# Kernel optimization log

Measured on AMD Instinct MI355X. Metric: run time of the kernel, lower is better.

Reference implementation:

```python
import jax, jax.numpy as jnp
import numpy as np

B, N = 256, 4096
IMG_W, IMG_H = 640.0, 480.0


def setup_inputs() -> dict:
    key = jax.random.key(0)
    k0, k1, k2, k3 = jax.random.split(key, 4)
    kpts0 = jax.random.uniform(k0, (B, N, 2), dtype=jnp.float32) * jnp.array([IMG_W, IMG_H], jnp.float32)
    kpts1 = jax.random.uniform(k1, (B, N, 2), dtype=jnp.float32) * jnp.array([IMG_W, IMG_H], jnp.float32)
    conf = jax.random.uniform(k2, (B, N, 1), dtype=jnp.float32)
    t_scale = jax.random.uniform(k3, (B, 2), dtype=jnp.float32) + 0.5
    Kmat = jnp.array([[500.0, 0.0, 320.0], [0.0, 500.0, 240.0], [0.0, 0.0, 1.0]], jnp.float32)
    K = jnp.tile(Kmat[None, None], (B, 2, 1, 1))
    gt_pose_0to1 = jnp.tile(jnp.eye(4, dtype=jnp.float32)[None], (B, 1, 1))
    return {"kpts0": kpts0, "kpts1": kpts1, "conf": conf, "t_scale": t_scale, "K": K, "gt_pose_0to1": gt_pose_0to1}


def _normalize(kpts, Kmat):
    # pixel -> normalized camera coords, homogeneous. kpts:[B,N,2], Kmat:[B,3,3] -> [B,N,3]
    Kinv = jnp.linalg.inv(Kmat)
    h = jnp.concatenate([kpts, jnp.ones_like(kpts[..., :1])], axis=-1)
    return jnp.einsum('bij,bnj->bni', Kinv, h)


def _se3_weighted_8pt(kpts0, kpts1, K0, K1, w, t_scale):
    b_, n_ = kpts0.shape[0], kpts0.shape[1]
    x0 = _normalize(kpts0, K0)  # [B,N,3]
    x1 = _normalize(kpts1, K1)  # [B,N,3]
    # epipolar constraint x1^T E x0 = 0 -> row kron(x1, x0): [B,N,9]
    X = (x1[..., :, None] * x0[..., None, :]).reshape(b_, n_, 9)
    # confidence-weighted normal equations, 9x9 per batch
    M = jnp.einsum('bn,bni,bnj->bij', w, X, X)
    _, V = jnp.linalg.eigh(M)
    E = V[..., 0].reshape(b_, 3, 3)  # eigvec of smallest eigenvalue
    # project to essential manifold + decompose
    U, S, Vt = jnp.linalg.svd(E)
    W = jnp.array([[0.0, -1.0, 0.0], [1.0, 0.0, 0.0], [0.0, 0.0, 1.0]], E.dtype)
    R1 = U @ W @ Vt
    R2 = U @ W.T @ Vt
    R1 = R1 * jnp.sign(jnp.linalg.det(R1))[:, None, None]
    R2 = R2 * jnp.sign(jnp.linalg.det(R2))[:, None, None]
    t = U[..., 2]  # [B,3]
    Rc = jnp.stack([R1, R1, R2, R2], axis=1)   # [B,4,3,3]
    tc = jnp.stack([t, -t, t, -t], axis=1)     # [B,4,3]
    # cheirality: solve d0 * (R x0) - d1 * x1 = -t in least squares (2x2 closed form)
    a = jnp.einsum('bcij,bnj->bcni', Rc, x0)   # [B,4,N,3]
    bvec = x1[:, None]                          # [B,1,N,3]
    tt = tc[:, :, None, :]                      # [B,4,1,3]
    aa = jnp.sum(a * a, -1)
    bb = jnp.sum(bvec * bvec, -1)
    ab = jnp.sum(a * bvec, -1)
    at = jnp.sum(a * tt, -1)
    bt = jnp.sum(bvec * tt, -1)
    det = aa * bb - ab * ab + 1e-9
    d0 = (-at * bb + ab * bt) / det
    d1 = (aa * bt - ab * at) / det
    pos = ((d0 > 0) & (d1 > 0)).astype(w.dtype)
    score = jnp.sum(w[:, None] * pos, -1)       # [B,4]
    best = jnp.argmax(jax.lax.stop_gradient(score), axis=-1)
    oh = jax.nn.one_hot(best, 4, dtype=kpts0.dtype)
    R = jnp.einsum('bc,bcij->bij', oh, Rc)
    t_best = jnp.einsum('bc,bci->bi', oh, tc)
    t_sc = t_best * t_scale[:, None]            # scale unit translation
    top = jnp.concatenate([R, t_sc[..., None]], axis=-1)  # [B,3,4]
    bot = jnp.broadcast_to(jnp.array([0.0, 0.0, 0.0, 1.0], R.dtype), (b_, 1, 4))
    return jnp.concatenate([top, bot], axis=1)  # [B,4,4]


def _se3_inverse(T):
    R = T[:, :3, :3]
    t = T[:, :3, 3:]
    Rt = jnp.swapaxes(R, -1, -2)
    tin = -(Rt @ t)
    top = jnp.concatenate([Rt, tin], axis=-1)
    bot = jnp.broadcast_to(jnp.array([0.0, 0.0, 0.0, 1.0], T.dtype), (T.shape[0], 1, 4))
    return jnp.concatenate([top, bot], axis=1)


def reference(kpts0, kpts1, conf, t_scale, K, gt_pose_0to1):
    w = conf[..., 0]
    T01 = _se3_weighted_8pt(kpts0, kpts1, K[:, 0], K[:, 1], w, t_scale[:, 0])
    T10 = _se3_inverse(T01)
    return jnp.stack([T01, T10], axis=1)  # [B,2,4,4]
```

## Files before the change

kernel.cpp:

```cpp
#include <hip/hip_runtime.h>
#include <math.h>

#define NBATCH 256
#define NPTS   4096
#define NT     256
#define PPT    (NPTS / NT)

__device__ __forceinline__ void inv3x3d(const float* __restrict__ Km, double* Ki) {
  double a = Km[0], bb = Km[1], c = Km[2];
  double d = Km[3], e  = Km[4], f = Km[5];
  double g = Km[6], h  = Km[7], i = Km[8];
  double C00 =  e*i - f*h;
  double C01 = -(d*i - f*g);
  double C02 =  d*h - e*g;
  double det = a*C00 + bb*C01 + c*C02;
  double rd = 1.0/det;
  Ki[0] = C00*rd; Ki[1] = -(bb*i - c*h)*rd; Ki[2] =  (bb*f - c*e)*rd;
  Ki[3] = C01*rd; Ki[4] =  (a*i  - c*g)*rd; Ki[5] = -(a*f  - c*d)*rd;
  Ki[6] = C02*rd; Ki[7] = -(a*h - bb*g)*rd; Ki[8] =  (a*e  - bb*d)*rd;
}

__global__ __launch_bounds__(NT, 1)
void pose_kernel(const float* __restrict__ kpts0,
                 const float* __restrict__ kpts1,
                 const float* __restrict__ conf,
                 const float* __restrict__ t_scale,
                 const float* __restrict__ Kmat,
                 float* __restrict__ out)
{
  const int b    = blockIdx.x;
  const int tid  = threadIdx.x;
  const int lane = tid & 63;
  const int wv   = tid >> 6;

  __shared__ double red[4][45];
  __shared__ double sM[45];
  __shared__ double sR[21];
  __shared__ double sscore[4][4];

  double Ki0[9], Ki1[9];
  inv3x3d(Kmat + (size_t)b*18,     Ki0);
  inv3x3d(Kmat + (size_t)b*18 + 9, Ki1);

  const float2* k0p = (const float2*)kpts0 + (size_t)b*NPTS;
  const float2* k1p = (const float2*)kpts1 + (size_t)b*NPTS;
  const float*  cp  = conf + (size_t)b*NPTS;

  double acc[45];
#pragma unroll
  for (int j=0;j<45;j++) acc[j] = 0.0;

  for (int p=0;p<PPT;p++) {
    const int i = tid + p*NT;
    const float2 q0 = k0p[i];
    const float2 q1 = k1p[i];
    const double w  = (double)cp[i];
    double x0[3], x1[3];
    x0[0] = Ki0[0]*q0.x + Ki0[1]*q0.y + Ki0[2];
    x0[1] = Ki0[3]*q0.x + Ki0[4]*q0.y + Ki0[5];
    x0[2] = Ki0[6]*q0.x + Ki0[7]*q0.y + Ki0[8];
    x1[0] = Ki1[0]*q1.x + Ki1[1]*q1.y + Ki1[2];
    x1[1] = Ki1[3]*q1.x + Ki1[4]*q1.y + Ki1[5];
    x1[2] = Ki1[6]*q1.x + Ki1[7]*q1.y + Ki1[8];
    double X[9];
#pragma unroll
    for (int ii=0; ii<3; ii++)
#pragma unroll
      for (int jj=0; jj<3; jj++)
        X[ii*3+jj] = x1[ii]*x0[jj];
    double wX[9];
#pragma unroll
    for (int j=0;j<9;j++) wX[j] = w*X[j];
    int k = 0;
#pragma unroll
    for (int r=0;r<9;r++)
#pragma unroll
      for (int c=r;c<9;c++) { acc[k] = fma(wX[r], X[c], acc[k]); k++; }
  }

#pragma unroll
  for (int j=0;j<45;j++) {
    double v = acc[j];
#pragma unroll
    for (int off=32; off>0; off>>=1) v += __shfl_xor(v, off, 64);
    acc[j] = v;
  }
  if (lane == 0) {
#pragma unroll
    for (int j=0;j<45;j++) red[wv][j] = acc[j];
  }
  __syncthreads();
  if (tid < 45) sM[tid] = red[0][tid] + red[1][tid] + red[2][tid] + red[3][tid];
  __syncthreads();

  double R1a[9] = {0}, R2a[9] = {0}, ta[3] = {0};
  if (tid == 0) {
    double A[9][9];
#pragma unroll
    for (int r=0;r<9;r++)
#pragma unroll
      for (int c=0;c<9;c++) {
        const int rr = (r<c)?r:c, cc = (r<c)?c:r;
        A[r][c] = sM[rr*9 - (rr*(rr-1))/2 + (cc-rr)];
      }
    double dinv[9];
#pragma unroll
    for (int k=0;k<9;k++) {
      double s = A[k][k];
#pragma unroll
      for (int j=0;j<k;j++) s -= A[k][j]*A[k][j];
      double l = sqrt(fmax(s, 1e-30));
      A[k][k] = l;
      dinv[k] = 1.0/l;
#pragma unroll
      for (int i2=k+1;i2<9;i2++) {
        double s2 = A[i2][k];
#pragma unroll
        for (int j=0;j<k;j++) s2 -= A[i2][j]*A[k][j];
        A[i2][k] = s2*dinv[k];
      }
    }
    double v[9];
#pragma unroll
    for (int j=0;j<9;j++) v[j] = 0.125;
    v[4] = 1.0;
    for (int it=0; it<24; it++) {
      double y[9], z[9];
#pragma unroll
      for (int i2=0;i2<9;i2++) {
        double s = v[i2];
#pragma unroll
        for (int j=0;j<i2;j++) s -= A[i2][j]*y[j];
        y[i2] = s*dinv[i2];
      }
#pragma unroll
      for (int i2=8;i2>=0;i2--) {
        double s = y[i2];
#pragma unroll
        for (int j=i2+1;j<9;j++) s -= A[j][i2]*z[j];
        z[i2] = s*dinv[i2];
      }
      double nn = 0.0;
#pragma unroll
      for (int j=0;j<9;j++) nn += z[j]*z[j];
      double rn = 1.0/sqrt(nn);
#pragma unroll
      for (int j=0;j<9;j++) v[j] = z[j]*rn;
    }
    double E0[3][3];
#pragma unroll
    for (int ii=0;ii<3;ii++)
#pragma unroll
      for (int jj=0;jj<3;jj++) E0[ii][jj] = v[ii*3+jj];
    double G[3][3];
#pragma unroll
    for (int a2=0;a2<3;a2++)
#pragma unroll
      for (int b2=0;b2<3;b2++)
        G[a2][b2] = E0[0][a2]*E0[0][b2] + E0[1][a2]*E0[1][b2] + E0[2][a2]*E0[2][b2];
    double Vv[3][3] = {{1,0,0},{0,1,0},{0,0,1}};
#define JROT(P,Q,RR) do { \
      double apq = G[P][Q]; \
      if (fabs(apq) > 1e-300) { \
        double app = G[P][P], aqq = G[Q][Q]; \
        double tau = (aqq - app) / (2.0*apq); \
        double tt = ((tau >= 0.0) ? 1.0 : -1.0) / (fabs(tau) + sqrt(1.0 + tau*tau)); \
        double cc_ = 1.0/sqrt(1.0 + tt*tt); \
        double ss_ = tt*cc_; \
        G[P][P] = app - tt*apq; \
        G[Q][Q] = aqq + tt*apq; \
        G[P][Q] = 0.0; G[Q][P] = 0.0; \
        double grp = G[RR][P], grq = G[RR][Q]; \
        G[RR][P] = cc_*grp - ss_*grq; G[P][RR] = G[RR][P]; \
        G[RR][Q] = ss_*grp + cc_*grq; G[Q][RR] = G[RR][Q]; \
        double v0p = Vv[0][P], v0q = Vv[0][Q]; \
        Vv[0][P] = cc_*v0p - ss_*v0q; Vv[0][Q] = ss_*v0p + cc_*v0q; \
        double v1p = Vv[1][P], v1q = Vv[1][Q]; \
        Vv[1][P] = cc_*v1p - ss_*v1q; Vv[1][Q] = ss_*v1p + cc_*v1q; \
        double v2p = Vv[2][P], v2q = Vv[2][Q]; \
        Vv[2][P] = cc_*v2p - ss_*v2q; Vv[2][Q] = ss_*v2p + cc_*v2q; \
      } } while(0)
    for (int sw=0; sw<8; sw++) { JROT(0,1,2); JROT(0,2,1); JROT(1,2,0); }
#undef JROT
    double lam[3] = {G[0][0], G[1][1], G[2][2]};
#define CSWAP(A_,B_) if (lam[A_] < lam[B_]) { \
      double tl = lam[A_]; lam[A_] = lam[B_]; lam[B_] = tl; \
      double t0_ = Vv[0][A_]; Vv[0][A_] = Vv[0][B_]; Vv[0][B_] = t0_; \
      double t1_ = Vv[1][A_]; Vv[1][A_] = Vv[1][B_]; Vv[1][B_] = t1_; \
      double t2_ = Vv[2][A_]; Vv[2][A_] = Vv[2][B_]; Vv[2][B_] = t2_; }
    CSWAP(0,1); CSWAP(0,2); CSWAP(1,2);
#undef CSWAP
    double u1[3], u2[3], u3[3];
#pragma unroll
    for (int i3=0;i3<3;i3++)
      u1[i3] = E0[i3][0]*Vv[0][0] + E0[i3][1]*Vv[1][0] + E0[i3][2]*Vv[2][0];
    double n1 = 1.0/sqrt(fmax(u1[0]*u1[0]+u1[1]*u1[1]+u1[2]*u1[2], 1e-300));
#pragma unroll
    for (int i3=0;i3<3;i3++) u1[i3] *= n1;
#pragma unroll
    for (int i3=0;i3<3;i3++)
      u2[i3] = E0[i3][0]*Vv[0][1] + E0[i3][1]*Vv[1][1] + E0[i3][2]*Vv[2][1];
    double d12 = u1[0]*u2[0]+u1[1]*u2[1]+u1[2]*u2[2];
#pragma unroll
    for (int i3=0;i3<3;i3++) u2[i3] -= d12*u1[i3];
    double n2 = 1.0/sqrt(fmax(u2[0]*u2[0]+u2[1]*u2[1]+u2[2]*u2[2], 1e-300));
#pragma unroll
    for (int i3=0;i3<3;i3++) u2[i3] *= n2;
    u3[0] = u1[1]*u2[2] - u1[2]*u2[1];
    u3[1] = u1[2]*u2[0] - u1[0]*u2[2];
    u3[2] = u1[0]*u2[1] - u1[1]*u2[0];
#pragma unroll
    for (int i3=0;i3<3;i3++)
#pragma unroll
      for (int j3=0;j3<3;j3++) {
        double m  = u3[i3]*Vv[j3][2];
        double pA = u2[i3]*Vv[j3][0] - u1[i3]*Vv[j3][1];
        R1a[i3*3+j3] = pA + m;
        R2a[i3*3+j3] = m - pA;
      }
    double det1 = R1a[0]*(R1a[4]*R1a[8]-R1a[5]*R1a[7])
                - R1a[1]*(R1a[3]*R1a[8]-R1a[5]*R1a[6])
                + R1a[2]*(R1a[3]*R1a[7]-R1a[4]*R1a[6]);
    double det2 = R2a[0]*(R2a[4]*R2a[8]-R2a[5]*R2a[7])
                - R2a[1]*(R2a[3]*R2a[8]-R2a[5]*R2a[6])
                + R2a[2]*(R2a[3]*R2a[7]-R2a[4]*R2a[6]);
    double sg1 = (det1 < 0.0) ? -1.0 : 1.0;
    double sg2 = (det2 < 0.0) ? -1.0 : 1.0;
#pragma unroll
    for (int j3=0;j3<9;j3++) { R1a[j3] *= sg1; R2a[j3] *= sg2; }
    ta[0] = u3[0]; ta[1] = u3[1]; ta[2] = u3[2];
#pragma unroll
    for (int j3=0;j3<9;j3++) { sR[j3] = R1a[j3]; sR[9+j3] = R2a[j3]; }
    sR[18] = ta[0]; sR[19] = ta[1]; sR[20] = ta[2];
  }
  __syncthreads();

  double r1[9], r2[9], tv3[3];
#pragma unroll
  for (int j=0;j<9;j++) { r1[j] = sR[j]; r2[j] = sR[9+j]; }
  tv3[0] = sR[18]; tv3[1] = sR[19]; tv3[2] = sR[20];

  double sc[4] = {0.0, 0.0, 0.0, 0.0};
  for (int p=0;p<PPT;p++) {
    const int i = tid + p*NT;
    const float2 q0 = k0p[i];
    const float2 q1 = k1p[i];
    const double w  = (double)cp[i];
    double x0[3], x1[3];
    x0[0] = Ki0[0]*q0.x + Ki0[1]*q0.y + Ki0[2];
    x0[1] = Ki0[3]*q0.x + Ki0[4]*q0.y + Ki0[5];
    x0[2] = Ki0[6]*q0.x + Ki0[7]*q0.y + Ki0[8];
    x1[0] = Ki1[0]*q1.x + Ki1[1]*q1.y + Ki1[2];
    x1[1] = Ki1[3]*q1.x + Ki1[4]*q1.y + Ki1[5];
    x1[2] = Ki1[6]*q1.x + Ki1[7]*q1.y + Ki1[8];
    const double bb2 = x1[0]*x1[0]+x1[1]*x1[1]+x1[2]*x1[2];
    const double bt  = x1[0]*tv3[0]+x1[1]*tv3[1]+x1[2]*tv3[2];
    {
      double a0 = r1[0]*x0[0]+r1[1]*x0[1]+r1[2]*x0[2];
      double a1 = r1[3]*x0[0]+r1[4]*x0[1]+r1[5]*x0[2];
      double a2 = r1[6]*x0[0]+r1[7]*x0[1]+r1[8]*x0[2];
      double aa = a0*a0+a1*a1+a2*a2;
      double ab = a0*x1[0]+a1*x1[1]+a2*x1[2];
      double at = a0*tv3[0]+a1*tv3[1]+a2*tv3[2];
      double n0v = ab*bt - at*bb2;
      double n1v = aa*bt - ab*at;
      if (n0v > 0.0 && n1v > 0.0) sc[0] += w;
      if (n0v < 0.0 && n1v < 0.0) sc[1] += w;
    }
    {
      double a0 = r2[0]*x0[0]+r2[1]*x0[1]+r2[2]*x0[2];
      double a1 = r2[3]*x0[0]+r2[4]*x0[1]+r2[5]*x0[2];
      double a2 = r2[6]*x0[0]+r2[7]*x0[1]+r2[8]*x0[2];
      double aa = a0*a0+a1*a1+a2*a2;
      double ab = a0*x1[0]+a1*x1[1]+a2*x1[2];
      double at = a0*tv3[0]+a1*tv3[1]+a2*tv3[2];
      double n0v = ab*bt - at*bb2;
      double n1v = aa*bt - ab*at;
      if (n0v > 0.0 && n1v > 0.0) sc[2] += w;
      if (n0v < 0.0 && n1v < 0.0) sc[3] += w;
    }
  }
#pragma unroll
  for (int c=0;c<4;c++) {
    double vv = sc[c];
#pragma unroll
    for (int off=32; off>0; off>>=1) vv += __shfl_xor(vv, off, 64);
    sc[c] = vv;
  }
  if (lane == 0) {
#pragma unroll
    for (int c=0;c<4;c++) sscore[wv][c] = sc[c];
  }
  __syncthreads();

  if (tid == 0) {
    double st0 = sscore[0][0]+sscore[1][0]+sscore[2][0]+sscore[3][0];
    double st1 = sscore[0][1]+sscore[1][1]+sscore[2][1]+sscore[3][1];
    double st2 = sscore[0][2]+sscore[1][2]+sscore[2][2]+sscore[3][2];
    double st3 = sscore[0][3]+sscore[1][3]+sscore[2][3]+sscore[3][3];
    int bestc = 0; double bs = st0;
    if (st1 > bs) { bs = st1; bestc = 1; }
    if (st2 > bs) { bs = st2; bestc = 2; }
    if (st3 > bs) { bs = st3; bestc = 3; }
    double Rb[9];
#pragma unroll
    for (int j=0;j<9;j++) Rb[j] = (bestc < 2) ? R1a[j] : R2a[j];
    const double sg = (bestc & 1) ? -1.0 : 1.0;
    const double ts = (double)t_scale[(size_t)b*2];
    const double t0 = sg*ta[0]*ts, t1 = sg*ta[1]*ts, t2 = sg*ta[2]*ts;
    float* o = out + (size_t)b*32;
    o[0]=(float)Rb[0]; o[1]=(float)Rb[1]; o[2] =(float)Rb[2]; o[3] =(float)t0;
    o[4]=(float)Rb[3]; o[5]=(float)Rb[4]; o[6] =(float)Rb[5]; o[7] =(float)t1;
    o[8]=(float)Rb[6]; o[9]=(float)Rb[7]; o[10]=(float)Rb[8]; o[11]=(float)t2;
    o[12]=0.f; o[13]=0.f; o[14]=0.f; o[15]=1.f;
    const double ti0 = -(Rb[0]*t0 + Rb[3]*t1 + Rb[6]*t2);
    const double ti1 = -(Rb[1]*t0 + Rb[4]*t1 + Rb[7]*t2);
    const double ti2 = -(Rb[2]*t0 + Rb[5]*t1 + Rb[8]*t2);
    o[16]=(float)Rb[0]; o[17]=(float)Rb[3]; o[18]=(float)Rb[6]; o[19]=(float)ti0;
    o[20]=(float)Rb[1]; o[21]=(float)Rb[4]; o[22]=(float)Rb[7]; o[23]=(float)ti1;
    o[24]=(float)Rb[2]; o[25]=(float)Rb[5]; o[26]=(float)Rb[8]; o[27]=(float)ti2;
    o[28]=0.f; o[29]=0.f; o[30]=0.f; o[31]=1.f;
  }
}

extern "C" void kernel_launch(void* const* d_in, const int* in_sizes, int n_in,
                              void* d_out, int out_size, void* d_ws, size_t ws_size,
                              hipStream_t stream) {
  (void)in_sizes; (void)n_in; (void)out_size; (void)d_ws; (void)ws_size;
  const float* kpts0   = (const float*)d_in[0];
  const float* kpts1   = (const float*)d_in[1];
  const float* conf    = (const float*)d_in[2];
  const float* tscale  = (const float*)d_in[3];
  const float* K       = (const float*)d_in[4];
  float* outp = (float*)d_out;
  pose_kernel<<<dim3(NBATCH), dim3(NT), 0, stream>>>(kpts0, kpts1, conf, tscale, K, outp);
}
```

Before: 110.9 us.

## Split pose kernel into reduce, batched solve, and score kernels in fp32

Splits the single fused kernel into three launches. The first builds the 9x9 normal matrix in fp32 with 512 threads per block. The second solves the eigen and SVD problem with one thread per batch, replacing the per-iteration triangular solves with an explicit inverse-matrix power iteration that runs fewer iterations and fewer Jacobi sweeps. The third scores cheirality in fp32. The aim is to move the point loops off slow fp64 arithmetic and to stop 255 threads idling during the serial solve, at the cost of extra launches, workspace traffic and lower numerical precision, since fp32 accumulation of the normal equations may hurt eigenvector accuracy.

```diff
diff --git a/kernel.cpp b/kernel.cpp
--- a/kernel.cpp
+++ b/kernel.cpp
@@ -3,8 +3,6 @@
 
 #define NBATCH 256
 #define NPTS   4096
-#define NT     256
-#define PPT    (NPTS / NT)
 
 __device__ __forceinline__ void inv3x3d(const float* __restrict__ Km, double* Ki) {
   double a = Km[0], bb = Km[1], c = Km[2];
@@ -20,269 +18,342 @@
   Ki[6] = C02*rd; Ki[7] = -(a*h - bb*g)*rd; Ki[8] =  (a*e  - bb*d)*rd;
 }
 
-__global__ __launch_bounds__(NT, 1)
-void pose_kernel(const float* __restrict__ kpts0,
-                 const float* __restrict__ kpts1,
-                 const float* __restrict__ conf,
-                 const float* __restrict__ t_scale,
-                 const float* __restrict__ Kmat,
-                 float* __restrict__ out)
+#define IDX(r,c)   ((r)*((r)+1)/2+(c))
+#define UPIDX(r,c) ((r)*9 - ((r)*((r)-1))/2 + ((c)-(r)))
+
+#define K1_T   512
+#define K1_PPT (NPTS / K1_T)
+
+__global__ __launch_bounds__(K1_T, 2)
+void k1_reduce(const float* __restrict__ kpts0,
+               const float* __restrict__ kpts1,
+               const float* __restrict__ conf,
+               const float* __restrict__ Kmat,
+               double* __restrict__ Mws)
 {
   const int b    = blockIdx.x;
   const int tid  = threadIdx.x;
   const int lane = tid & 63;
   const int wv   = tid >> 6;
 
-  __shared__ double red[4][45];
-  __shared__ double sM[45];
-  __shared__ double sR[21];
-  __shared__ double sscore[4][4];
-
-  double Ki0[9], Ki1[9];
-  inv3x3d(Kmat + (size_t)b*18,     Ki0);
-  inv3x3d(Kmat + (size_t)b*18 + 9, Ki1);
+  __shared__ double red[K1_T/64][45];
+
+  double Kd[9];
+  float Ki0[9], Ki1[9];
+  inv3x3d(Kmat + (size_t)b*18, Kd);
+#pragma unroll
+  for (int j=0;j<9;j++) Ki0[j] = (float)Kd[j];
+  inv3x3d(Kmat + (size_t)b*18 + 9, Kd);
+#pragma unroll
+  for (int j=0;j<9;j++) Ki1[j] = (float)Kd[j];
 
   const float2* k0p = (const float2*)kpts0 + (size_t)b*NPTS;
   const float2* k1p = (const float2*)kpts1 + (size_t)b*NPTS;
   const float*  cp  = conf + (size_t)b*NPTS;
 
-  double acc[45];
-#pragma unroll
-  for (int j=0;j<45;j++) acc[j] = 0.0;
-
-  for (int p=0;p<PPT;p++) {
-    const int i = tid + p*NT;
+  float acc[45];
+#pragma unroll
+  for (int j=0;j<45;j++) acc[j] = 0.f;
+
+  for (int p=0;p<K1_PPT;p++) {
+    const int i = tid + p*K1_T;
     const float2 q0 = k0p[i];
     const float2 q1 = k1p[i];
-    const double w  = (double)cp[i];
-    double x0[3], x1[3];
-    x0[0] = Ki0[0]*q0.x + Ki0[1]*q0.y + Ki0[2];
-    x0[1] = Ki0[3]*q0.x + Ki0[4]*q0.y + Ki0[5];
-    x0[2] = Ki0[6]*q0.x + Ki0[7]*q0.y + Ki0[8];
-    x1[0] = Ki1[0]*q1.x + Ki1[1]*q1.y + Ki1[2];
-    x1[1] = Ki1[3]*q1.x + Ki1[4]*q1.y + Ki1[5];
-    x1[2] = Ki1[6]*q1.x + Ki1[7]*q1.y + Ki1[8];
-    double X[9];
+    const float  w  = cp[i];
+    float x0[3], x1[3];
+    x0[0] = fmaf(Ki0[0],q0.x, fmaf(Ki0[1],q0.y, Ki0[2]));
+    x0[1] = fmaf(Ki0[3],q0.x, fmaf(Ki0[4],q0.y, Ki0[5]));
+    x0[2] = fmaf(Ki0[6],q0.x, fmaf(Ki0[7],q0.y, Ki0[8]));
+    x1[0] = fmaf(Ki1[0],q1.x, fmaf(Ki1[1],q1.y, Ki1[2]));
+    x1[1] = fmaf(Ki1[3],q1.x, fmaf(Ki1[4],q1.y, Ki1[5]));
+    x1[2] = fmaf(Ki1[6],q1.x, fmaf(Ki1[7],q1.y, Ki1[8]));
+    float X[9], wX[9];
 #pragma unroll
     for (int ii=0; ii<3; ii++)
 #pragma unroll
       for (int jj=0; jj<3; jj++)
         X[ii*3+jj] = x1[ii]*x0[jj];
-    double wX[9];
 #pragma unroll
     for (int j=0;j<9;j++) wX[j] = w*X[j];
     int k = 0;
 #pragma unroll
     for (int r=0;r<9;r++)
 #pragma unroll
-      for (int c=r;c<9;c++) { acc[k] = fma(wX[r], X[c], acc[k]); k++; }
+      for (int c=r;c<9;c++) { acc[k] = fmaf(wX[r], X[c], acc[k]); k++; }
   }
 
 #pragma unroll
   for (int j=0;j<45;j++) {
-    double v = acc[j];
+    float v = acc[j];
 #pragma unroll
     for (int off=32; off>0; off>>=1) v += __shfl_xor(v, off, 64);
     acc[j] = v;
   }
   if (lane == 0) {
 #pragma unroll
-    for (int j=0;j<45;j++) red[wv][j] = acc[j];
+    for (int j=0;j<45;j++) red[wv][j] = (double)acc[j];
   }
   __syncthreads();
-  if (tid < 45) sM[tid] = red[0][tid] + red[1][tid] + red[2][tid] + red[3][tid];
-  __syncthreads();
-
-  double R1a[9] = {0}, R2a[9] = {0}, ta[3] = {0};
-  if (tid == 0) {
-    double A[9][9];
-#pragma unroll
-    for (int r=0;r<9;r++)
-#pragma unroll
-      for (int c=0;c<9;c++) {
-        const int rr = (r<c)?r:c, cc = (r<c)?c:r;
-        A[r][c] = sM[rr*9 - (rr*(rr-1))/2 + (cc-rr)];
+  if (tid < 45) {
+    double s = 0.0;
+#pragma unroll
+    for (int wq=0; wq<K1_T/64; wq++) s += red[wq][tid];
+    Mws[(size_t)b*45 + tid] = s;
+  }
+}
+
+__global__ __launch_bounds__(64, 1)
+void k2_solve(const double* __restrict__ Mws,
+              float* __restrict__ Rws)
+{
+  const int b = blockIdx.x*64 + threadIdx.x;
+  const double* Mb = Mws + (size_t)b*45;
+
+  double L[45];
+#pragma unroll
+  for (int r=0;r<9;r++)
+#pragma unroll
+    for (int c=0;c<=r;c++)
+      L[IDX(r,c)] = Mb[UPIDX(c,r)];
+
+  double dinv[9];
+#pragma unroll
+  for (int k=0;k<9;k++) {
+    double s = L[IDX(k,k)];
+#pragma unroll
+    for (int j=0;j<k;j++) s -= L[IDX(k,j)]*L[IDX(k,j)];
+    double l = sqrt(fmax(s, 1e-30));
+    L[IDX(k,k)] = l;
+    dinv[k] = 1.0/l;
+#pragma unroll
+    for (int i2=k+1;i2<9;i2++) {
+      double s2 = L[IDX(i2,k)];
+#pragma unroll
+      for (int j=0;j<k;j++) s2 -= L[IDX(i2,j)]*L[IDX(k,j)];
+      L[IDX(i2,k)] = s2*dinv[k];
+    }
+  }
+
+  double W[45];
+#pragma unroll
+  for (int j=0;j<9;j++) {
+    W[IDX(j,j)] = dinv[j];
+#pragma unroll
+    for (int i2=j+1;i2<9;i2++) {
+      double s = 0.0;
+#pragma unroll
+      for (int k=j;k<i2;k++) s += L[IDX(i2,k)]*W[IDX(k,j)];
+      W[IDX(i2,j)] = -s*dinv[i2];
+    }
+  }
+
+  double Bm[45];
+#pragma unroll
+  for (int i2=0;i2<9;i2++)
+#pragma unroll
+    for (int j=0;j<=i2;j++) {
+      double s = 0.0;
+#pragma unroll
+      for (int k=i2;k<9;k++) s += W[IDX(k,i2)]*W[IDX(k,j)];
+      Bm[IDX(i2,j)] = s;
+    }
+
+  double v[9];
+#pragma unroll
+  for (int j=0;j<9;j++) v[j] = 0.125;
+  v[4] = 1.0;
+  for (int it=0; it<20; it++) {
+    double y[9];
+#pragma unroll
+    for (int i2=0;i2<9;i2++) {
+      double s = 0.0;
+#pragma unroll
+      for (int j=0;j<9;j++) {
+        const int rr = (i2>j)?i2:j, cc = (i2>j)?j:i2;
+        s = fma(Bm[IDX(rr,cc)], v[j], s);
       }
-    double dinv[9];
-#pragma unroll
-    for (int k=0;k<9;k++) {
-      double s = A[k][k];
-#pragma unroll
-      for (int j=0;j<k;j++) s -= A[k][j]*A[k][j];
-      double l = sqrt(fmax(s, 1e-30));
-      A[k][k] = l;
-      dinv[k] = 1.0/l;
-#pragma unroll
-      for (int i2=k+1;i2<9;i2++) {
-        double s2 = A[i2][k];
-#pragma unroll
-        for (int j=0;j<k;j++) s2 -= A[i2][j]*A[k][j];
-        A[i2][k] = s2*dinv[k];
-      }
-    }
-    double v[9];
-#pragma unroll
-    for (int j=0;j<9;j++) v[j] = 0.125;
-    v[4] = 1.0;
-    for (int it=0; it<24; it++) {
-      double y[9], z[9];
-#pragma unroll
-      for (int i2=0;i2<9;i2++) {
-        double s = v[i2];
-#pragma unroll
-        for (int j=0;j<i2;j++) s -= A[i2][j]*y[j];
-        y[i2] = s*dinv[i2];
-      }
-#pragma unroll
-      for (int i2=8;i2>=0;i2--) {
-        double s = y[i2];
-#pragma unroll
-        for (int j=i2+1;j<9;j++) s -= A[j][i2]*z[j];
-        z[i2] = s*dinv[i2];
-      }
-      double nn = 0.0;
-#pragma unroll
-      for (int j=0;j<9;j++) nn += z[j]*z[j];
-      double rn = 1.0/sqrt(nn);
-#pragma unroll
-      for (int j=0;j<9;j++) v[j] = z[j]*rn;
-    }
-    double E0[3][3];
-#pragma unroll
-    for (int ii=0;ii<3;ii++)
-#pragma unroll
-      for (int jj=0;jj<3;jj++) E0[ii][jj] = v[ii*3+jj];
-    double G[3][3];
-#pragma unroll
-    for (int a2=0;a2<3;a2++)
-#pragma unroll
-      for (int b2=0;b2<3;b2++)
-        G[a2][b2] = E0[0][a2]*E0[0][b2] + E0[1][a2]*E0[1][b2] + E0[2][a2]*E0[2][b2];
-    double Vv[3][3] = {{1,0,0},{0,1,0},{0,0,1}};
+      y[i2] = s;
+    }
+#pragma unroll
+    for (int j=0;j<9;j++) v[j] = y[j];
+  }
+  {
+    double nn = 0.0;
+#pragma unroll
+    for (int j=0;j<9;j++) nn += v[j]*v[j];
+    double rn = 1.0/sqrt(nn);
+#pragma unroll
+    for (int j=0;j<9;j++) v[j] *= rn;
+  }
+
+  double E0[3][3];
+#pragma unroll
+  for (int ii=0;ii<3;ii++)
+#pragma unroll
+    for (int jj=0;jj<3;jj++) E0[ii][jj] = v[ii*3+jj];
+  double G[3][3];
+#pragma unroll
+  for (int a2=0;a2<3;a2++)
+#pragma unroll
+    for (int b2=0;b2<3;b2++)
+      G[a2][b2] = E0[0][a2]*E0[0][b2] + E0[1][a2]*E0[1][b2] + E0[2][a2]*E0[2][b2];
+  double Vv[3][3] = {{1,0,0},{0,1,0},{0,0,1}};
 #define JROT(P,Q,RR) do { \
-      double apq = G[P][Q]; \
-      if (fabs(apq) > 1e-300) { \
-        double app = G[P][P], aqq = G[Q][Q]; \
-        double tau = (aqq - app) / (2.0*apq); \
-        double tt = ((tau >= 0.0) ? 1.0 : -1.0) / (fabs(tau) + sqrt(1.0 + tau*tau)); \
-        double cc_ = 1.0/sqrt(1.0 + tt*tt); \
-        double ss_ = tt*cc_; \
-        G[P][P] = app - tt*apq; \
-        G[Q][Q] = aqq + tt*apq; \
-        G[P][Q] = 0.0; G[Q][P] = 0.0; \
-        double grp = G[RR][P], grq = G[RR][Q]; \
-        G[RR][P] = cc_*grp - ss_*grq; G[P][RR] = G[RR][P]; \
-        G[RR][Q] = ss_*grp + cc_*grq; G[Q][RR] = G[RR][Q]; \
-        double v0p = Vv[0][P], v0q = Vv[0][Q]; \
-        Vv[0][P] = cc_*v0p - ss_*v0q; Vv[0][Q] = ss_*v0p + cc_*v0q; \
-        double v1p = Vv[1][P], v1q = Vv[1][Q]; \
-        Vv[1][P] = cc_*v1p - ss_*v1q; Vv[1][Q] = ss_*v1p + cc_*v1q; \
-        double v2p = Vv[2][P], v2q = Vv[2][Q]; \
-        Vv[2][P] = cc_*v2p - ss_*v2q; Vv[2][Q] = ss_*v2p + cc_*v2q; \
-      } } while(0)
-    for (int sw=0; sw<8; sw++) { JROT(0,1,2); JROT(0,2,1); JROT(1,2,0); }
+    double apq = G[P][Q]; \
+    if (fabs(apq) > 1e-300) { \
+      double app = G[P][P], aqq = G[Q][Q]; \
+      double tau = (aqq - app) / (2.0*apq); \
+      double tt = ((tau >= 0.0) ? 1.0 : -1.0) / (fabs(tau) + sqrt(1.0 + tau*tau)); \
+      double cc_ = 1.0/sqrt(1.0 + tt*tt); \
+      double ss_ = tt*cc_; \
+      G[P][P] = app - tt*apq; \
+      G[Q][Q] = aqq + tt*apq; \
+      G[P][Q] = 0.0; G[Q][P] = 0.0; \
+      double grp = G[RR][P], grq = G[RR][Q]; \
+      G[RR][P] = cc_*grp - ss_*grq; G[P][RR] = G[RR][P]; \
+      G[RR][Q] = ss_*grp + cc_*grq; G[Q][RR] = G[RR][Q]; \
+      double v0p = Vv[0][P], v0q = Vv[0][Q]; \
+      Vv[0][P] = cc_*v0p - ss_*v0q; Vv[0][Q] = ss_*v0p + cc_*v0q; \
+      double v1p = Vv[1][P], v1q = Vv[1][Q]; \
+      Vv[1][P] = cc_*v1p - ss_*v1q; Vv[1][Q] = ss_*v1p + cc_*v1q; \
+      double v2p = Vv[2][P], v2q = Vv[2][Q]; \
+      Vv[2][P] = cc_*v2p - ss_*v2q; Vv[2][Q] = ss_*v2p + cc_*v2q; \
+    } } while(0)
+  for (int sw=0; sw<6; sw++) { JROT(0,1,2); JROT(0,2,1); JROT(1,2,0); }
 #undef JROT
-    double lam[3] = {G[0][0], G[1][1], G[2][2]};
+  double lam[3] = {G[0][0], G[1][1], G[2][2]};
 #define CSWAP(A_,B_) if (lam[A_] < lam[B_]) { \
-      double tl = lam[A_]; lam[A_] = lam[B_]; lam[B_] = tl; \
-      double t0_ = Vv[0][A_]; Vv[0][A_] = Vv[0][B_]; Vv[0][B_] = t0_; \
-      double t1_ = Vv[1][A_]; Vv[1][A_] = Vv[1][B_]; Vv[1][B_] = t1_; \
-      double t2_ = Vv[2][A_]; Vv[2][A_] = Vv[2][B_]; Vv[2][B_] = t2_; }
-    CSWAP(0,1); CSWAP(0,2); CSWAP(1,2);
+    double tl = lam[A_]; lam[A_] = lam[B_]; lam[B_] = tl; \
+    double t0_ = Vv[0][A_]; Vv[0][A_] = Vv[0][B_]; Vv[0][B_] = t0_; \
+    double t1_ = Vv[1][A_]; Vv[1][A_] = Vv[1][B_]; Vv[1][B_] = t1_; \
+    double t2_ = Vv[2][A_]; Vv[2][A_] = Vv[2][B_]; Vv[2][B_] = t2_; }
+  CSWAP(0,1); CSWAP(0,2); CSWAP(1,2);
 #undef CSWAP
-    double u1[3], u2[3], u3[3];
-#pragma unroll
-    for (int i3=0;i3<3;i3++)
-      u1[i3] = E0[i3][0]*Vv[0][0] + E0[i3][1]*Vv[1][0] + E0[i3][2]*Vv[2][0];
-    double n1 = 1.0/sqrt(fmax(u1[0]*u1[0]+u1[1]*u1[1]+u1[2]*u1[2], 1e-300));
-#pragma unroll
-    for (int i3=0;i3<3;i3++) u1[i3] *= n1;
-#pragma unroll
-    for (int i3=0;i3<3;i3++)
-      u2[i3] = E0[i3][0]*Vv[0][1] + E0[i3][1]*Vv[1][1] + E0[i3][2]*Vv[2][1];
-    double d12 = u1[0]*u2[0]+u1[1]*u2[1]+u1[2]*u2[2];
-#pragma unroll
-    for (int i3=0;i3<3;i3++) u2[i3] -= d12*u1[i3];
-    double n2 = 1.0/sqrt(fmax(u2[0]*u2[0]+u2[1]*u2[1]+u2[2]*u2[2], 1e-300));
-#pragma unroll
-    for (int i3=0;i3<3;i3++) u2[i3] *= n2;
-    u3[0] = u1[1]*u2[2] - u1[2]*u2[1];
-    u3[1] = u1[2]*u2[0] - u1[0]*u2[2];
-    u3[2] = u1[0]*u2[1] - u1[1]*u2[0];
-#pragma unroll
-    for (int i3=0;i3<3;i3++)
-#pragma unroll
-      for (int j3=0;j3<3;j3++) {
-        double m  = u3[i3]*Vv[j3][2];
-        double pA = u2[i3]*Vv[j3][0] - u1[i3]*Vv[j3][1];
-        R1a[i3*3+j3] = pA + m;
-        R2a[i3*3+j3] = m - pA;
-      }
-    double det1 = R1a[0]*(R1a[4]*R1a[8]-R1a[5]*R1a[7])
-                - R1a[1]*(R1a[3]*R1a[8]-R1a[5]*R1a[6])
-                + R1a[2]*(R1a[3]*R1a[7]-R1a[4]*R1a[6]);
-    double det2 = R2a[0]*(R2a[4]*R2a[8]-R2a[5]*R2a[7])
-                - R2a[1]*(R2a[3]*R2a[8]-R2a[5]*R2a[6])
-                + R2a[2]*(R2a[3]*R2a[7]-R2a[4]*R2a[6]);
-    double sg1 = (det1 < 0.0) ? -1.0 : 1.0;
-    double sg2 = (det2 < 0.0) ? -1.0 : 1.0;
-#pragma unroll
-    for (int j3=0;j3<9;j3++) { R1a[j3] *= sg1; R2a[j3] *= sg2; }
-    ta[0] = u3[0]; ta[1] = u3[1]; ta[2] = u3[2];
-#pragma unroll
-    for (int j3=0;j3<9;j3++) { sR[j3] = R1a[j3]; sR[9+j3] = R2a[j3]; }
-    sR[18] = ta[0]; sR[19] = ta[1]; sR[20] = ta[2];
-  }
-  __syncthreads();
-
-  double r1[9], r2[9], tv3[3];
-#pragma unroll
-  for (int j=0;j<9;j++) { r1[j] = sR[j]; r2[j] = sR[9+j]; }
-  tv3[0] = sR[18]; tv3[1] = sR[19]; tv3[2] = sR[20];
-
-  double sc[4] = {0.0, 0.0, 0.0, 0.0};
-  for (int p=0;p<PPT;p++) {
-    const int i = tid + p*NT;
+  double u1[3], u2[3], u3[3];
+#pragma unroll
+  for (int i3=0;i3<3;i3++)
+    u1[i3] = E0[i3][0]*Vv[0][0] + E0[i3][1]*Vv[1][0] + E0[i3][2]*Vv[2][0];
+  double n1 = 1.0/sqrt(fmax(u1[0]*u1[0]+u1[1]*u1[1]+u1[2]*u1[2], 1e-300));
+#pragma unroll
+  for (int i3=0;i3<3;i3++) u1[i3] *= n1;
+#pragma unroll
+  for (int i3=0;i3<3;i3++)
+    u2[i3] = E0[i3][0]*Vv[0][1] + E0[i3][1]*Vv[1][1] + E0[i3][2]*Vv[2][1];
+  double d12 = u1[0]*u2[0]+u1[1]*u2[1]+u1[2]*u2[2];
+#pragma unroll
+  for (int i3=0;i3<3;i3++) u2[i3] -= d12*u1[i3];
+  double n2 = 1.0/sqrt(fmax(u2[0]*u2[0]+u2[1]*u2[1]+u2[2]*u2[2], 1e-300));
+#pragma unroll
+  for (int i3=0;i3<3;i3++) u2[i3] *= n2;
+  u3[0] = u1[1]*u2[2] - u1[2]*u2[1];
+  u3[1] = u1[2]*u2[0] - u1[0]*u2[2];
+  u3[2] = u1[0]*u2[1] - u1[1]*u2[0];
+  double R1a[9], R2a[9];
+#pragma unroll
+  for (int i3=0;i3<3;i3++)
+#pragma unroll
+    for (int j3=0;j3<3;j3++) {
+      double m  = u3[i3]*Vv[j3][2];
+      double pA = u2[i3]*Vv[j3][0] - u1[i3]*Vv[j3][1];
+      R1a[i3*3+j3] = pA + m;
+      R2a[i3*3+j3] = m - pA;
+    }
+  double det1 = R1a[0]*(R1a[4]*R1a[8]-R1a[5]*R1a[7])
+              - R1a[1]*(R1a[3]*R1a[8]-R1a[5]*R1a[6])
+              + R1a[2]*(R1a[3]*R1a[7]-R1a[4]*R1a[6]);
+  double det2 = R2a[0]*(R2a[4]*R2a[8]-R2a[5]*R2a[7])
+              - R2a[1]*(R2a[3]*R2a[8]-R2a[5]*R2a[6])
+              + R2a[2]*(R2a[3]*R2a[7]-R2a[4]*R2a[6]);
+  double sg1 = (det1 < 0.0) ? -1.0 : 1.0;
+  double sg2 = (det2 < 0.0) ? -1.0 : 1.0;
+
+  float* o = Rws + (size_t)b*21;
+#pragma unroll
+  for (int j=0;j<9;j++) { o[j] = (float)(sg1*R1a[j]); o[9+j] = (float)(sg2*R2a[j]); }
+  o[18] = (float)u3[0]; o[19] = (float)u3[1]; o[20] = (float)u3[2];
+}
+
+#define K3_T   512
+#define K3_PPT (NPTS / K3_T)
+
+__global__ __launch_bounds__(K3_T, 2)
+void k3_score(const float* __restrict__ kpts0,
+              const float* __restrict__ kpts1,
+              const float* __restrict__ conf,
+              const float* __restrict__ t_scale,
+              const float* __restrict__ Kmat,
+              const float* __restrict__ Rws,
+              float* __restrict__ out)
+{
+  const int b    = blockIdx.x;
+  const int tid  = threadIdx.x;
+  const int lane = tid & 63;
+  const int wv   = tid >> 6;
+
+  __shared__ float sscore[K3_T/64][4];
+
+  double Kd[9];
+  float Ki0[9], Ki1[9];
+  inv3x3d(Kmat + (size_t)b*18, Kd);
+#pragma unroll
+  for (int j=0;j<9;j++) Ki0[j] = (float)Kd[j];
+  inv3x3d(Kmat + (size_t)b*18 + 9, Kd);
+#pragma unroll
+  for (int j=0;j<9;j++) Ki1[j] = (float)Kd[j];
+
+  const float* rb = Rws + (size_t)b*21;
+  float r1[9], r2[9], tv[3];
+#pragma unroll
+  for (int j=0;j<9;j++) { r1[j] = rb[j]; r2[j] = rb[9+j]; }
+  tv[0] = rb[18]; tv[1] = rb[19]; tv[2] = rb[20];
+
+  const float2* k0p = (const float2*)kpts0 + (size_t)b*NPTS;
+  const float2* k1p = (const float2*)kpts1 + (size_t)b*NPTS;
+  const float*  cp  = conf + (size_t)b*NPTS;
+
+  float sc[4] = {0.f, 0.f, 0.f, 0.f};
+  for (int p=0;p<K3_PPT;p++) {
+    const int i = tid + p*K3_T;
     const float2 q0 = k0p[i];
     const float2 q1 = k1p[i];
-    const double w  = (double)cp[i];
-    double x0[3], x1[3];
-    x0[0] = Ki0[0]*q0.x + Ki0[1]*q0.y + Ki0[2];
-    x0[1] = Ki0[3]*q0.x + Ki0[4]*q0.y + Ki0[5];
-    x0[2] = Ki0[6]*q0.x + Ki0[7]*q0.y + Ki0[8];
-    x1[0] = Ki1[0]*q1.x + Ki1[1]*q1.y + Ki1[2];
-    x1[1] = Ki1[3]*q1.x + Ki1[4]*q1.y + Ki1[5];
-    x1[2] = Ki1[6]*q1.x + Ki1[7]*q1.y + Ki1[8];
-    const double bb2 = x1[0]*x1[0]+x1[1]*x1[1]+x1[2]*x1[2];
-    const double bt  = x1[0]*tv3[0]+x1[1]*tv3[1]+x1[2]*tv3[2];
+    const float  w  = cp[i];
+    float x0[3], x1[3];
+    x0[0] = fmaf(Ki0[0],q0.x, fmaf(Ki0[1],q0.y, Ki0[2]));
+    x0[1] = fmaf(Ki0[3],q0.x, fmaf(Ki0[4],q0.y, Ki0[5]));
+    x0[2] = fmaf(Ki0[6],q0.x, fmaf(Ki0[7],q0.y, Ki0[8]));
+    x1[0] = fmaf(Ki1[0],q1.x, fmaf(Ki1[1],q1.y, Ki1[2]));
+    x1[1] = fmaf(Ki1[3],q1.x, fmaf(Ki1[4],q1.y, Ki1[5]));
+    x1[2] = fmaf(Ki1[6],q1.x, fmaf(Ki1[7],q1.y, Ki1[8]));
+    const float bb2 = x1[0]*x1[0]+x1[1]*x1[1]+x1[2]*x1[2];
+    const float bt  = x1[0]*tv[0]+x1[1]*tv[1]+x1[2]*tv[2];
     {
-      double a0 = r1[0]*x0[0]+r1[1]*x0[1]+r1[2]*x0[2];
-      double a1 = r1[3]*x0[0]+r1[4]*x0[1]+r1[5]*x0[2];
-      double a2 = r1[6]*x0[0]+r1[7]*x0[1]+r1[8]*x0[2];
-      double aa = a0*a0+a1*a1+a2*a2;
-      double ab = a0*x1[0]+a1*x1[1]+a2*x1[2];
-      double at = a0*tv3[0]+a1*tv3[1]+a2*tv3[2];
-      double n0v = ab*bt - at*bb2;
-      double n1v = aa*bt - ab*at;
-      if (n0v > 0.0 && n1v > 0.0) sc[0] += w;
-      if (n0v < 0.0 && n1v < 0.0) sc[1] += w;
+      float a0 = r1[0]*x0[0]+r1[1]*x0[1]+r1[2]*x0[2];
+      float a1 = r1[3]*x0[0]+r1[4]*x0[1]+r1[5]*x0[2];
+      float a2 = r1[6]*x0[0]+r1[7]*x0[1]+r1[8]*x0[2];
+      float aa = a0*a0+a1*a1+a2*a2;
+      float ab = a0*x1[0]+a1*x1[1]+a2*x1[2];
+      float at = a0*tv[0]+a1*tv[1]+a2*tv[2];
+      float n0v = ab*bt - at*bb2;
+      float n1v = aa*bt - ab*at;
+      if (n0v > 0.f && n1v > 0.f) sc[0] += w;
+      if (n0v < 0.f && n1v < 0.f) sc[1] += w;
     }
     {
-      double a0 = r2[0]*x0[0]+r2[1]*x0[1]+r2[2]*x0[2];
-      double a1 = r2[3]*x0[0]+r2[4]*x0[1]+r2[5]*x0[2];
-      double a2 = r2[6]*x0[0]+r2[7]*x0[1]+r2[8]*x0[2];
-      double aa = a0*a0+a1*a1+a2*a2;
-      double ab = a0*x1[0]+a1*x1[1]+a2*x1[2];
-      double at = a0*tv3[0]+a1*tv3[1]+a2*tv3[2];
-      double n0v = ab*bt - at*bb2;
-      double n1v = aa*bt - ab*at;
-      if (n0v > 0.0 && n1v > 0.0) sc[2] += w;
-      if (n0v < 0.0 && n1v < 0.0) sc[3] += w;
+      float a0 = r2[0]*x0[0]+r2[1]*x0[1]+r2[2]*x0[2];
+      float a1 = r2[3]*x0[0]+r2[4]*x0[1]+r2[5]*x0[2];
+      float a2 = r2[6]*x0[0]+r2[7]*x0[1]+r2[8]*x0[2];
+      float aa = a0*a0+a1*a1+a2*a2;
+      float ab = a0*x1[0]+a1*x1[1]+a2*x1[2];
+      float at = a0*tv[0]+a1*tv[1]+a2*tv[2];
+      float n0v = ab*bt - at*bb2;
+      float n1v = aa*bt - ab*at;
+      if (n0v > 0.f && n1v > 0.f) sc[2] += w;
+      if (n0v < 0.f && n1v < 0.f) sc[3] += w;
     }
   }
 #pragma unroll
   for (int c=0;c<4;c++) {
-    double vv = sc[c];
+    float vv = sc[c];
 #pragma unroll
     for (int off=32; off>0; off>>=1) vv += __shfl_xor(vv, off, 64);
     sc[c] = vv;
@@ -294,31 +365,35 @@
   __syncthreads();
 
   if (tid == 0) {
-    double st0 = sscore[0][0]+sscore[1][0]+sscore[2][0]+sscore[3][0];
-    double st1 = sscore[0][1]+sscore[1][1]+sscore[2][1]+sscore[3][1];
-    double st2 = sscore[0][2]+sscore[1][2]+sscore[2][2]+sscore[3][2];
-    double st3 = sscore[0][3]+sscore[1][3]+sscore[2][3]+sscore[3][3];
-    int bestc = 0; double bs = st0;
-    if (st1 > bs) { bs = st1; bestc = 1; }
-    if (st2 > bs) { bs = st2; bestc = 2; }
-    if (st3 > bs) { bs = st3; bestc = 3; }
-    double Rb[9];
-#pragma unroll
-    for (int j=0;j<9;j++) Rb[j] = (bestc < 2) ? R1a[j] : R2a[j];
-    const double sg = (bestc & 1) ? -1.0 : 1.0;
-    const double ts = (double)t_scale[(size_t)b*2];
-    const double t0 = sg*ta[0]*ts, t1 = sg*ta[1]*ts, t2 = sg*ta[2]*ts;
+    float st[4];
+#pragma unroll
+    for (int c=0;c<4;c++) {
+      float s = 0.f;
+#pragma unroll
+      for (int wq=0; wq<K3_T/64; wq++) s += sscore[wq][c];
+      st[c] = s;
+    }
+    int bestc = 0; float bs = st[0];
+    if (st[1] > bs) { bs = st[1]; bestc = 1; }
+    if (st[2] > bs) { bs = st[2]; bestc = 2; }
+    if (st[3] > bs) { bs = st[3]; bestc = 3; }
+    float Rb[9];
+#pragma unroll
+    for (int j=0;j<9;j++) Rb[j] = (bestc < 2) ? r1[j] : r2[j];
+    const float sg = (bestc & 1) ? -1.f : 1.f;
+    const float ts = t_scale[(size_t)b*2];
+    const float t0 = sg*tv[0]*ts, t1 = sg*tv[1]*ts, t2 = sg*tv[2]*ts;
     float* o = out + (size_t)b*32;
-    o[0]=(float)Rb[0]; o[1]=(float)Rb[1]; o[2] =(float)Rb[2]; o[3] =(float)t0;
-    o[4]=(float)Rb[3]; o[5]=(float)Rb[4]; o[6] =(float)Rb[5]; o[7] =(float)t1;
-    o[8]=(float)Rb[6]; o[9]=(float)Rb[7]; o[10]=(float)Rb[8]; o[11]=(float)t2;
+    o[0]=Rb[0]; o[1]=Rb[1]; o[2] =Rb[2]; o[3] =t0;
+    o[4]=Rb[3]; o[5]=Rb[4]; o[6] =Rb[5]; o[7] =t1;
+    o[8]=Rb[6]; o[9]=Rb[7]; o[10]=Rb[8]; o[11]=t2;
     o[12]=0.f; o[13]=0.f; o[14]=0.f; o[15]=1.f;
-    const double ti0 = -(Rb[0]*t0 + Rb[3]*t1 + Rb[6]*t2);
-    const double ti1 = -(Rb[1]*t0 + Rb[4]*t1 + Rb[7]*t2);
-    const double ti2 = -(Rb[2]*t0 + Rb[5]*t1 + Rb[8]*t2);
-    o[16]=(float)Rb[0]; o[17]=(float)Rb[3]; o[18]=(float)Rb[6]; o[19]=(float)ti0;
-    o[20]=(float)Rb[1]; o[21]=(float)Rb[4]; o[22]=(float)Rb[7]; o[23]=(float)ti1;
-    o[24]=(float)Rb[2]; o[25]=(float)Rb[5]; o[26]=(float)Rb[8]; o[27]=(float)ti2;
+    const float ti0 = -(Rb[0]*t0 + Rb[3]*t1 + Rb[6]*t2);
+    const float ti1 = -(Rb[1]*t0 + Rb[4]*t1 + Rb[7]*t2);
+    const float ti2 = -(Rb[2]*t0 + Rb[5]*t1 + Rb[8]*t2);
+    o[16]=Rb[0]; o[17]=Rb[3]; o[18]=Rb[6]; o[19]=ti0;
+    o[20]=Rb[1]; o[21]=Rb[4]; o[22]=Rb[7]; o[23]=ti1;
+    o[24]=Rb[2]; o[25]=Rb[5]; o[26]=Rb[8]; o[27]=ti2;
     o[28]=0.f; o[29]=0.f; o[30]=0.f; o[31]=1.f;
   }
 }
@@ -326,12 +401,18 @@
 extern "C" void kernel_launch(void* const* d_in, const int* in_sizes, int n_in,
                               void* d_out, int out_size, void* d_ws, size_t ws_size,
                               hipStream_t stream) {
-  (void)in_sizes; (void)n_in; (void)out_size; (void)d_ws; (void)ws_size;
-  const float* kpts0   = (const float*)d_in[0];
-  const float* kpts1   = (const float*)d_in[1];
-  const float* conf    = (const float*)d_in[2];
-  const float* tscale  = (const float*)d_in[3];
-  const float* K       = (const float*)d_in[4];
+  (void)in_sizes; (void)n_in; (void)out_size; (void)ws_size;
+  const float* kpts0  = (const float*)d_in[0];
+  const float* kpts1  = (const float*)d_in[1];
+  const float* conf   = (const float*)d_in[2];
+  const float* tscale = (const float*)d_in[3];
+  const float* K      = (const float*)d_in[4];
   float* outp = (float*)d_out;
-  pose_kernel<<<dim3(NBATCH), dim3(NT), 0, stream>>>(kpts0, kpts1, conf, tscale, K, outp);
+
+  double* Mws = (double*)d_ws;
+  float*  Rws = (float*)((char*)d_ws + (size_t)NBATCH*45*8);
+
+  k1_reduce<<<dim3(NBATCH), dim3(K1_T), 0, stream>>>(kpts0, kpts1, conf, K, Mws);
+  k2_solve <<<dim3(NBATCH/64), dim3(64), 0, stream>>>(Mws, Rws);
+  k3_score <<<dim3(NBATCH), dim3(K3_T), 0, stream>>>(kpts0, kpts1, conf, tscale, K, Rws, outp);
 }
```

After: 101.8 us. 8.2% less time.
